# Optimization experiments

Hardware: AMD Instinct MI355X
Metric: run time of the kernel (lower is better)

## Reference

```python
import jax, jax.numpy as jnp
import numpy as np

HID = 1024   # hidden_size
NH = 16      # num_heads
NKV = 4      # num_kv_heads
HD = 64      # head_dim
C = 64       # chunk_size
RATIO = 0.125  # freq_cutoff_ratio
KS = 7       # conv_kernel_size


def setup_inputs() -> dict:
    key = jax.random.key(0)
    ks = jax.random.split(key, 11)
    B, N = 4, 4096
    s = 0.02
    return {
        "hidden_states": jax.random.normal(ks[0], (B, N, HID), jnp.float32),
        "q_w": jax.random.normal(ks[1], (NH * HD, HID), jnp.float32) * s,
        "k_w": jax.random.normal(ks[2], (NKV * HD, HID), jnp.float32) * s,
        "v_w": jax.random.normal(ks[3], (NKV * HD, HID), jnp.float32) * s,
        "o_w": jax.random.normal(ks[4], (HID, NH * HD), jnp.float32) * s,
        "dw_r": jax.random.normal(ks[5], (HID, 1, KS), jnp.float32) * 0.3,
        "pw_r": jax.random.normal(ks[6], (HID, HID), jnp.float32) * s,
        "dw_i": jax.random.normal(ks[7], (HID, 1, KS), jnp.float32) * 0.3,
        "pw_i": jax.random.normal(ks[8], (HID, HID), jnp.float32) * s,
        "gate_w": jax.random.normal(ks[9], (HID, HID), jnp.float32) * s,
        "alpha_raw": jnp.zeros((1,), jnp.float32),
    }


def _block_causal_attention(x, qw, kw, vw, ow, k):
    # x: [B, nc, k, D] real. Flatten chunk freq bins; chunk j attends to chunks 0..j.
    B, nc, _, D = x.shape
    T = nc * k
    xf = x.reshape(B, T, D)
    q = (xf @ qw.T).reshape(B, T, NH, HD).transpose(0, 2, 1, 3)    # [B,H,T,hd]
    kk = (xf @ kw.T).reshape(B, T, NKV, HD).transpose(0, 2, 1, 3)
    v = (xf @ vw.T).reshape(B, T, NKV, HD).transpose(0, 2, 1, 3)
    rep = NH // NKV
    kk = jnp.repeat(kk, rep, axis=1)
    v = jnp.repeat(v, rep, axis=1)
    chunk_ids = jnp.arange(T) // k
    mask = chunk_ids[:, None] >= chunk_ids[None, :]                # [T,T] bool
    scores = jnp.einsum('bhqd,bhkd->bhqk', q, kk) / np.float32(np.sqrt(HD))
    scores = jnp.where(mask[None, None], scores, jnp.finfo(scores.dtype).min)
    p = jax.nn.softmax(scores, axis=-1)
    o = jnp.einsum('bhqk,bhkd->bhqd', p, v)
    o = o.transpose(0, 2, 1, 3).reshape(B, T, NH * HD)
    return (o @ ow.T).reshape(B, nc, k, D)


def _causal_conv(x, dw, pw):
    # x: [B, nc, L, D] real. Depthwise causal conv + GELU + pointwise conv.
    B, nc, L, D = x.shape
    xc = x.reshape(B * nc, L, D).transpose(0, 2, 1)                # [BN, D, L]
    xp = jnp.pad(xc, ((0, 0), (0, 0), (KS - 1, 0)))                # causal left pad
    y = jax.lax.conv_general_dilated(
        xp, dw, window_strides=(1,), padding='VALID',
        dimension_numbers=('NCH', 'OIH', 'NCH'), feature_group_count=D)
    y = jax.nn.gelu(y, approximate=False)
    y = jnp.einsum('ncl,oc->nol', y, pw)                           # 1x1 conv
    return y.transpose(0, 2, 1).reshape(B, nc, L, D)


def _forward(hidden_states, q_w, k_w, v_w, o_w, dw_r, pw_r, dw_i, pw_i, gate_w, alpha_raw):
    B, N, D = hidden_states.shape
    pad_len = (-N) % C
    x = jnp.pad(hidden_states, ((0, 0), (0, pad_len), (0, 0))) if pad_len else hidden_states
    nc = x.shape[1] // C
    chunks = x.reshape(B, nc, C, D)
    Xh = jnp.fft.rfft(chunks.astype(jnp.float32), axis=2)          # [B,nc,M,D] complex
    M = Xh.shape[2]
    k = max(1, int(M * RATIO))
    X_low, X_high = Xh[:, :, :k, :], Xh[:, :, k:, :]
    # low-freq: block-causal attention on real and imag parts separately
    A_r = _block_causal_attention(X_low.real, q_w, k_w, v_w, o_w, k)
    A_i = _block_causal_attention(X_low.imag, q_w, k_w, v_w, o_w, k)
    A_low = jax.lax.complex(A_r, A_i)
    # high-freq: causal conv branch, gated by per-chunk time-domain mean
    H_r = _causal_conv(X_high.real, dw_r, pw_r)
    H_i = _causal_conv(X_high.imag, dw_i, pw_i)
    g = jax.nn.sigmoid(chunks.mean(axis=2) @ gate_w.T)[:, :, None, :]  # [B,nc,1,D]
    A_high = jax.lax.complex(H_r * g, H_i * g) + X_high
    alpha = jax.nn.sigmoid(alpha_raw)                               # [1]
    A_low_fused = alpha * A_low + (1.0 - alpha) * X_low
    Y_hat = jnp.concatenate([A_low_fused, A_high], axis=2)
    Y = jnp.fft.irfft(Y_hat, n=C, axis=2)
    return Y.reshape(B, -1, D)[:, :N, :].astype(hidden_states.dtype)


def reference(hidden_states, q_w, k_w, v_w, o_w, dw_r, pw_r, dw_i, pw_i, gate_w, alpha_raw):
    return _forward(hidden_states, q_w, k_w, v_w, o_w, dw_r, pw_r, dw_i, pw_i, gate_w, alpha_raw)
```

## Files before the change

### kernel.cpp

```cpp
#include <hip/hip_runtime.h>
#include <math.h>


typedef __bf16 bf16_t;
typedef bf16_t bf16x8 __attribute__((ext_vector_type(8)));
typedef float f32x4 __attribute__((ext_vector_type(4)));

#define EP_NONE 0
#define EP_SIGMOID 1
#define EP_FUSELOW 2
#define EP_HIGH 3

__device__ __forceinline__ void gld_lds16(const bf16_t* g, bf16_t* l) {
  __builtin_amdgcn_global_load_lds(
      (const __attribute__((address_space(1))) unsigned int*)g,
      (__attribute__((address_space(3))) unsigned int*)l, 16, 0, 0);
}

__global__ __launch_bounds__(256) void prep_w(
    const float* __restrict__ qw, const float* __restrict__ kw,
    const float* __restrict__ vw, const float* __restrict__ ow,
    const float* __restrict__ gw, const float* __restrict__ pwr,
    const float* __restrict__ pwi, bf16_t* __restrict__ Wqkv,
    bf16_t* __restrict__ owb, bf16_t* __restrict__ gwb,
    bf16_t* __restrict__ pwrb, bf16_t* __restrict__ pwib) {
  int gi = blockIdx.x * 256 + threadIdx.x;
  float4 v;
  bf16_t* o;
  if (gi < 393216) {
    if (gi < 262144) v = ((const float4*)qw)[gi];
    else if (gi < 327680) v = ((const float4*)kw)[gi - 262144];
    else v = ((const float4*)vw)[gi - 327680];
    o = Wqkv + (long)gi * 4;
  } else {
    int j = gi - 393216;
    int sel = j >> 18, off = j & 262143;
    const float* s = sel == 0 ? ow : sel == 1 ? gw : sel == 2 ? pwr : pwi;
    bf16_t* d = sel == 0 ? owb : sel == 1 ? gwb : sel == 2 ? pwrb : pwib;
    v = ((const float4*)s)[off];
    o = d + (long)off * 4;
  }
  o[0] = (bf16_t)v.x; o[1] = (bf16_t)v.y; o[2] = (bf16_t)v.z; o[3] = (bf16_t)v.w;
}

__global__ __launch_bounds__(256) void mk_basis(bf16_t* __restrict__ dhi,
                                                bf16_t* __restrict__ dres,
                                                bf16_t* __restrict__ bhi,
                                                bf16_t* __restrict__ bres,
                                                float* __restrict__ tlow) {
  int idx = blockIdx.x * 256 + threadIdx.x;
  const float TW = 6.283185307179586f / 64.f;
  if (idx < 5120) {
    int r = idx >> 6, k = idx & 63;
    float v = 0.f;
    if (r < 33) {
      v = cosf(TW * (float)((r * k) & 63));
    } else if (r < 66) {
      v = -sinf(TW * (float)(((r - 33) * k) & 63));
    }
    bf16_t h = (bf16_t)v;
    float res = v - (float)h;
    dhi[idx] = h;
    dres[idx] = (bf16_t)res;
  } else if (idx < 9216) {
    int i = idx - 5120;
    int t = i >> 6, k = i & 63;
    float v = 0.f;
    if (k < 28) {
      int ft = ((4 + k) * t) & 63;
      v = 2.f * cosf(TW * (float)ft) * (1.f / 64.f);
    } else if (k == 28) {
      int ft = (32 * t) & 63;
      v = cosf(TW * (float)ft) * (1.f / 64.f);
    } else if (k < 57) {
      int ft = ((k - 25) * t) & 63;
      v = -2.f * sinf(TW * (float)ft) * (1.f / 64.f);
    }
    bf16_t h = (bf16_t)v;
    float res = v - (float)h;
    bhi[i] = h;
    bres[i] = (bf16_t)res;
  } else if (idx < 9728) {
    int i = idx - 9216;
    int t = i >> 3, j = i & 7;
    float v = 0.f;
    if (j == 0) v = 1.f / 64.f;
    else if (j < 7) {
      int f = (j + 1) >> 1;
      int ft = (f * t) & 63;
      float th = TW * (float)ft;
      v = (j & 1) ? 2.f * cosf(th) * (1.f / 64.f)
                  : -2.f * sinf(th) * (1.f / 64.f);
    }
    tlow[i] = v;
  }
}

__global__ __launch_bounds__(128) void dft_mfma(
    const float* __restrict__ X, const bf16_t* __restrict__ dhi,
    const bf16_t* __restrict__ dres, bf16_t* __restrict__ Xh,
    bf16_t* __restrict__ XLr, bf16_t* __restrict__ XLi,
    bf16_t* __restrict__ gmean) {
  const int bc = blockIdx.y;
  const int d0 = blockIdx.x * 128;
  const int tid = threadIdx.x;
  const int lane = tid & 63, wave = tid >> 6;
  const int mr = lane & 15, q = lane >> 4;
  const int wn = wave * 64;

  __shared__ bf16_t Bh[128 * 64];
  __shared__ bf16_t Br[128 * 64];

  {
    const float* xc = X + ((long)bc * 64) * 1024 + d0 + tid;
    float xv[64];
#pragma unroll
    for (int t = 0; t < 64; t++) xv[t] = xc[(long)t * 1024];
    const int sw = tid & 7;
#pragma unroll
    for (int g = 0; g < 8; g++) {
      bf16x8 vh, vr;
#pragma unroll
      for (int i = 0; i < 8; i++) {
        float v = xv[g * 8 + i];
        bf16_t h = (bf16_t)v;
        vh[i] = h;
        vr[i] = (bf16_t)(v - (float)h);
      }
      *(bf16x8*)&Bh[tid * 64 + ((g ^ sw) << 3)] = vh;
      *(bf16x8*)&Br[tid * 64 + ((g ^ sw) << 3)] = vr;
    }
  }
  __syncthreads();

  f32x4 acc[5][4];
#pragma unroll
  for (int i = 0; i < 5; i++)
#pragma unroll
    for (int j = 0; j < 4; j++) acc[i][j] = (f32x4){0.f, 0.f, 0.f, 0.f};

#pragma unroll
  for (int s = 0; s < 2; s++) {
    bf16x8 bh[4], br[4];
#pragma unroll
    for (int ni = 0; ni < 4; ni++) {
      int dcol = wn + ni * 16 + mr;
      int so = (((s * 4 + q) ^ (dcol & 7)) << 3);
      bh[ni] = *(const bf16x8*)&Bh[dcol * 64 + so];
      br[ni] = *(const bf16x8*)&Br[dcol * 64 + so];
    }
#pragma unroll
    for (int mi = 0; mi < 5; mi++) {
      int trow = mi * 16 + mr;
      bf16x8 ah = *(const bf16x8*)&dhi[trow * 64 + (s * 4 + q) * 8];
      bf16x8 ar = *(const bf16x8*)&dres[trow * 64 + (s * 4 + q) * 8];
#pragma unroll
      for (int ni = 0; ni < 4; ni++) {
        acc[mi][ni] = __builtin_amdgcn_mfma_f32_16x16x32_bf16(
            ah, bh[ni], acc[mi][ni], 0, 0, 0);
        acc[mi][ni] = __builtin_amdgcn_mfma_f32_16x16x32_bf16(
            ah, br[ni], acc[mi][ni], 0, 0, 0);
        acc[mi][ni] = __builtin_amdgcn_mfma_f32_16x16x32_bf16(
            ar, bh[ni], acc[mi][ni], 0, 0, 0);
      }
    }
  }

  const int b = bc >> 6, ch = bc & 63;
  bf16_t* xp = Xh + (long)bc * 66 * 1024 + d0;
#pragma unroll
  for (int mi = 0; mi < 5; mi++) {
#pragma unroll
    for (int r = 0; r < 4; r++) {
      int row = mi * 16 + q * 4 + r;
      if (row >= 66) continue;
#pragma unroll
      for (int ni = 0; ni < 4; ni++) {
        int col = wn + ni * 16 + mr;
        float val = acc[mi][ni][r];
        xp[(long)row * 1024 + col] = (bf16_t)val;
        if (row == 0)
          gmean[(long)bc * 1024 + d0 + col] = (bf16_t)(val * (1.f / 64.f));
        if (row < 4)
          XLr[((long)(b * 256 + ch * 4 + row)) * 1024 + d0 + col] = (bf16_t)val;
        if (row >= 33 && row < 37)
          XLi[((long)(b * 256 + ch * 4 + row - 33)) * 1024 + d0 + col] =
              (bf16_t)val;
      }
    }
  }
}

template <int EMODE>
__global__ __launch_bounds__(256, 2) void gemm128(
    const bf16_t* __restrict__ A0, const bf16_t* __restrict__ A1,
    const bf16_t* __restrict__ B0, const bf16_t* __restrict__ B1,
    int N, int ntc, int zc,
    void* __restrict__ C0v, void* __restrict__ C1v,
    const bf16_t* __restrict__ E0, const bf16_t* __restrict__ E1,
    const float* __restrict__ alpha_ptr) {
  constexpr int K = 1024;
  constexpr int NT = 32;
  __shared__ bf16_t lds[4][2][128 * 32];

  const int nwg = gridDim.x;
  const int g = (blockIdx.x & 7) * (nwg >> 3) + (blockIdx.x >> 3);
  const int per_mt = ntc * zc;
  const int mt = g / per_mt, rem = g - mt * per_mt;
  const int nt = rem % ntc, z = rem / ntc;
  const bf16_t* A = z ? A1 : A0;
  const bf16_t* B = z ? B1 : B0;
  void* Cv = z ? C1v : C0v;
  const bf16_t* E = z ? E1 : E0;
  const int m0 = mt * 128, n0 = nt * 128;

  const int tid = threadIdx.x;
  const int lane = tid & 63, wave = tid >> 6;
  const int wm = (wave & 1) * 64, wn = (wave >> 1) * 64;
  const int q = lane >> 4, mr = lane & 15;
  const int srow = tid >> 2, sk8 = (tid & 3) * 8;

  f32x4 acc[4][4];
#pragma unroll
  for (int i = 0; i < 4; i++)
#pragma unroll
    for (int j = 0; j < 4; j++) acc[i][j] = (f32x4){0.f, 0.f, 0.f, 0.f};

  auto stage = [&](int t) {
    const int bi = t & 3;
    const int kb = t * 32;
#pragma unroll
    for (int it = 0; it < 2; it++) {
      gld_lds16(A + (long)(m0 + it * 64 + srow) * K + kb + sk8,
                &lds[bi][0][(it * 256 + wave * 64) * 8]);
      gld_lds16(B + (long)(n0 + it * 64 + srow) * K + kb + sk8,
                &lds[bi][1][(it * 256 + wave * 64) * 8]);
    }
  };

  stage(0);
  stage(1);
  stage(2);

  for (int t = 0; t < NT; t++) {
    if (t < NT - 2)
      asm volatile("s_waitcnt vmcnt(8)" ::: "memory");
    else if (t == NT - 2)
      asm volatile("s_waitcnt vmcnt(4)" ::: "memory");
    else
      asm volatile("s_waitcnt vmcnt(0)" ::: "memory");
    __builtin_amdgcn_sched_barrier(0);
    __builtin_amdgcn_s_barrier();
    if (t + 3 < NT) stage(t + 3);

    const bf16_t* As_ = &lds[t & 3][0][0];
    const bf16_t* Bs_ = &lds[t & 3][1][0];
    bf16x8 bfr[4];
#pragma unroll
    for (int ni = 0; ni < 4; ni++)
      bfr[ni] = *(const bf16x8*)&Bs_[(wn + ni * 16 + mr) * 32 + q * 8];
    __builtin_amdgcn_s_setprio(1);
#pragma unroll
    for (int mi = 0; mi < 4; mi++) {
      bf16x8 af = *(const bf16x8*)&As_[(wm + mi * 16 + mr) * 32 + q * 8];
#pragma unroll
      for (int ni = 0; ni < 4; ni++)
        acc[mi][ni] = __builtin_amdgcn_mfma_f32_16x16x32_bf16(
            af, bfr[ni], acc[mi][ni], 0, 0, 0);
    }
    __builtin_amdgcn_s_setprio(0);
  }

  float alpha = 0.f;
  if constexpr (EMODE == EP_FUSELOW) alpha = 1.f / (1.f + __expf(-alpha_ptr[0]));
#pragma unroll
  for (int mi = 0; mi < 4; mi++) {
#pragma unroll
    for (int ni = 0; ni < 4; ni++) {
      int col = n0 + wn + ni * 16 + mr;
      int rbase = m0 + wm + mi * 16 + q * 4;
#pragma unroll
      for (int r = 0; r < 4; r++) {
        int row = rbase + r;
        float val = acc[mi][ni][r];
        if constexpr (EMODE == EP_NONE) {
          ((bf16_t*)Cv)[(long)row * N + col] = (bf16_t)val;
        } else if constexpr (EMODE == EP_SIGMOID) {
          ((float*)Cv)[(long)row * N + col] = 1.f / (1.f + __expf(-val));
        } else {
          float xl = (float)E[(long)row * 1024 + col];
          ((float*)Cv)[(long)row * 1024 + col] = alpha * val + (1.f - alpha) * xl;
        }
      }
    }
  }
}

__global__ __launch_bounds__(512, 2) void gemm256_high(
    const bf16_t* __restrict__ A0, const bf16_t* __restrict__ A1,
    const bf16_t* __restrict__ B0, const bf16_t* __restrict__ B1,
    bf16_t* __restrict__ XhMut, const float* __restrict__ gate) {
  constexpr int K = 1024;
  constexpr int NT = K / 32;
  __shared__ bf16_t lds[4][2][256 * 32];

  const int id = blockIdx.x;
  const int kk = (id & 7) * 29 + (id >> 3);
  const int mt = kk >> 3, rem = kk & 7;
  const int nt = rem & 3, z = rem >> 2;
  const bf16_t* A = z ? A1 : A0;
  const bf16_t* B = z ? B1 : B0;
  const int imoff = z ? 33 * 1024 : 0;
  const int m0 = mt * 256, n0 = nt * 256;

  const int tid = threadIdx.x;
  const int lane = tid & 63, wave = tid >> 6;
  const int wm = (wave & 1) * 128, wn = (wave >> 1) * 64;
  const int q = lane >> 4, mr = lane & 15;
  const int srow = tid >> 2;
  const int gk8 = (((tid & 3) ^ ((((tid >> 2) & 3) + ((tid >> 4) & 3)) & 3)) << 3);

  f32x4 acc[8][4];
#pragma unroll
  for (int i = 0; i < 8; i++)
#pragma unroll
    for (int j = 0; j < 4; j++) acc[i][j] = (f32x4){0.f, 0.f, 0.f, 0.f};

  auto stage = [&](int t) {
    const int bi = t & 3;
    const int kb = t * 32;
#pragma unroll
    for (int rd = 0; rd < 2; rd++) {
      gld_lds16(A + (long)(m0 + rd * 128 + srow) * K + kb + gk8,
                &lds[bi][0][(rd * 512 + wave * 64) * 8]);
      gld_lds16(B + (long)(n0 + rd * 128 + srow) * K + kb + gk8,
                &lds[bi][1][(rd * 512 + wave * 64) * 8]);
    }
  };

  stage(0);
  stage(1);
  stage(2);

  const int asl = (q ^ (((mr & 3) + ((mr >> 2) & 3)) & 3)) * 8;

  for (int t = 0; t < NT; t++) {
    if (t < NT - 2)
      asm volatile("s_waitcnt vmcnt(8)" ::: "memory");
    else if (t == NT - 2)
      asm volatile("s_waitcnt vmcnt(4)" ::: "memory");
    else
      asm volatile("s_waitcnt vmcnt(0)" ::: "memory");
    __builtin_amdgcn_sched_barrier(0);
    __builtin_amdgcn_s_barrier();
    if (t + 3 < NT) stage(t + 3);

    const bf16_t* As_ = &lds[t & 3][0][0];
    const bf16_t* Bs_ = &lds[t & 3][1][0];
    bf16x8 bfr[4];
#pragma unroll
    for (int ni = 0; ni < 4; ni++)
      bfr[ni] = *(const bf16x8*)&Bs_[(wn + ni * 16 + mr) * 32 + asl];
    __builtin_amdgcn_s_setprio(1);
#pragma unroll
    for (int mi = 0; mi < 8; mi++) {
      bf16x8 af = *(const bf16x8*)&As_[(wm + mi * 16 + mr) * 32 + asl];
#pragma unroll
      for (int ni = 0; ni < 4; ni++)
        acc[mi][ni] = __builtin_amdgcn_mfma_f32_16x16x32_bf16(
            af, bfr[ni], acc[mi][ni], 0, 0, 0);
    }
    __builtin_amdgcn_s_setprio(0);
  }

#pragma unroll
  for (int mi = 0; mi < 8; mi++) {
#pragma unroll
    for (int r = 0; r < 4; r++) {
      int row = m0 + wm + mi * 16 + q * 4 + r;
      int bc = row / 29, l = row - bc * 29;
      long xbase = ((long)bc * 66 + 4 + l) * 1024 + imoff;
      const float* gp = gate + (long)bc * 1024;
#pragma unroll
      for (int ni = 0; ni < 4; ni++) {
        int col = n0 + wn + ni * 16 + mr;
        long x = xbase + col;
        XhMut[x] = (bf16_t)fmaf(acc[mi][ni][r], gp[col], (float)XhMut[x]);
      }
    }
  }
}

__global__ __launch_bounds__(256) void attn_mfma(const bf16_t* __restrict__ QKVr,
                                                 const bf16_t* __restrict__ QKVi,
                                                 bf16_t* __restrict__ Or_,
                                                 bf16_t* __restrict__ Oi_) {
  const int h = blockIdx.x;
  const int b = blockIdx.y >> 2, qt = blockIdx.y & 3;
  const bf16_t* QKV = blockIdx.z ? QKVi : QKVr;
  bf16_t* O = blockIdx.z ? Oi_ : Or_;
  const int kvh = h >> 2;
  const int tid = threadIdx.x;
  const int lane = tid & 63, wave = tid >> 6;
  const int mr = lane & 15, q4 = lane >> 4;

  __shared__ bf16_t Ks[64 * 72];
  __shared__ bf16_t Vt[64 * 72];
  __shared__ bf16_t Ps[4][16 * 72];

  bf16x8 af[2];
  {
    const bf16_t* qp =
        QKV + (long)(b * 256 + qt * 64 + wave * 16 + mr) * 1536 + h * 64;
    af[0] = *(const bf16x8*)(qp + q4 * 8);
    af[1] = *(const bf16x8*)(qp + 32 + q4 * 8);
  }
  f32x4 Oacc[4];
#pragma unroll
  for (int ni = 0; ni < 4; ni++) Oacc[ni] = (f32x4){0.f, 0.f, 0.f, 0.f};
  float mrow[4], lrow[4];
#pragma unroll
  for (int r = 0; r < 4; r++) { mrow[r] = -1e30f; lrow[r] = 0.f; }

  for (int kt = 0; kt <= qt; kt++) {
#pragma unroll
    for (int it = 0; it < 2; it++) {
      int idx = tid + it * 256;
      int key = idx >> 3, dg = idx & 7;
      const bf16_t* kp = QKV + (long)(b * 256 + kt * 64 + key) * 1536 + 1024 +
                         kvh * 64 + dg * 8;
      *(bf16x8*)&Ks[key * 72 + dg * 8] = *(const bf16x8*)kp;
      bf16x8 vv = *(const bf16x8*)(kp + 256);
#pragma unroll
      for (int j = 0; j < 8; j++) Vt[(dg * 8 + j) * 72 + key] = vv[j];
    }
    __syncthreads();

    f32x4 S[4];
#pragma unroll
    for (int ni = 0; ni < 4; ni++) {
      S[ni] = (f32x4){0.f, 0.f, 0.f, 0.f};
#pragma unroll
      for (int s = 0; s < 2; s++) {
        bf16x8 kb = *(const bf16x8*)&Ks[(ni * 16 + mr) * 72 + s * 32 + q4 * 8];
        S[ni] = __builtin_amdgcn_mfma_f32_16x16x32_bf16(af[s], kb, S[ni], 0, 0, 0);
      }
    }
#pragma unroll
    for (int ni = 0; ni < 4; ni++) {
#pragma unroll
      for (int r = 0; r < 4; r++) {
        float v = S[ni][r] * 0.125f;
        if (kt == qt) {
          int qrow = wave * 16 + q4 * 4 + r;
          int kcol = ni * 16 + mr;
          if ((qrow >> 2) < (kcol >> 2)) v = -1e30f;
        }
        S[ni][r] = v;
      }
    }
#pragma unroll
    for (int r = 0; r < 4; r++) {
      float mx = fmaxf(fmaxf(S[0][r], S[1][r]), fmaxf(S[2][r], S[3][r]));
#pragma unroll
      for (int off = 1; off < 16; off <<= 1) mx = fmaxf(mx, __shfl_xor(mx, off));
      float mn = fmaxf(mrow[r], mx);
      float sc = __expf(mrow[r] - mn);
      mrow[r] = mn;
      float rs = 0.f;
#pragma unroll
      for (int ni = 0; ni < 4; ni++) {
        float p = __expf(S[ni][r] - mn);
        rs += p;
        Ps[wave][(q4 * 4 + r) * 72 + ni * 16 + mr] = (bf16_t)p;
      }
#pragma unroll
      for (int off = 1; off < 16; off <<= 1) rs += __shfl_xor(rs, off);
      lrow[r] = lrow[r] * sc + rs;
#pragma unroll
      for (int ni = 0; ni < 4; ni++) Oacc[ni][r] *= sc;
    }
    bf16x8 pa[2];
    pa[0] = *(const bf16x8*)&Ps[wave][mr * 72 + q4 * 8];
    pa[1] = *(const bf16x8*)&Ps[wave][mr * 72 + 32 + q4 * 8];
#pragma unroll
    for (int ni = 0; ni < 4; ni++) {
#pragma unroll
      for (int s = 0; s < 2; s++) {
        bf16x8 vb = *(const bf16x8*)&Vt[(ni * 16 + mr) * 72 + s * 32 + q4 * 8];
        Oacc[ni] = __builtin_amdgcn_mfma_f32_16x16x32_bf16(pa[s], vb, Oacc[ni], 0, 0, 0);
      }
    }
    __syncthreads();
  }

#pragma unroll
  for (int r = 0; r < 4; r++) {
    float inv = 1.f / lrow[r];
    long row = b * 256 + qt * 64 + wave * 16 + q4 * 4 + r;
#pragma unroll
    for (int ni = 0; ni < 4; ni++)
      O[row * 1024 + h * 64 + ni * 16 + mr] = (bf16_t)(Oacc[ni][r] * inv);
  }
}

__global__ __launch_bounds__(256) void dwconv_kernel(const bf16_t* __restrict__ Xh,
                                                     const float* __restrict__ dwr,
                                                     const float* __restrict__ dwi,
                                                     bf16_t* __restrict__ Gr,
                                                     bf16_t* __restrict__ Gi) {
  const int d = blockIdx.x * 256 + threadIdx.x;
  const int bc = blockIdx.y;
  const float* dw = blockIdx.z ? dwi : dwr;
  bf16_t* G = blockIdx.z ? Gi : Gr;
  const int imoff = blockIdx.z ? 33 * 1024 : 0;
  float w[7];
#pragma unroll
  for (int j = 0; j < 7; j++) w[j] = dw[d * 7 + j];
  float x[29];
#pragma unroll
  for (int l = 0; l < 29; l++)
    x[l] = (float)Xh[((long)bc * 66 + 4 + l) * 1024 + imoff + d];
#pragma unroll
  for (int l = 0; l < 29; l++) {
    float y = 0.f;
#pragma unroll
    for (int j = 0; j < 7; j++) {
      int src = l - 6 + j;
      if (src >= 0) y = fmaf(w[j], x[src], y);
    }
    float ge = 0.5f * y * (1.f + erff(y * 0.7071067811865475f));
    G[((long)bc * 29 + l) * 1024 + d] = (bf16_t)ge;
  }
}

__global__ __launch_bounds__(128) void irfft_mfma(
    const bf16_t* __restrict__ Xh, const float* __restrict__ Afr,
    const float* __restrict__ Afi, const bf16_t* __restrict__ bhi,
    const bf16_t* __restrict__ bres, const float* __restrict__ tlow,
    float* __restrict__ out) {
  const int bc = blockIdx.y;
  const int d0 = blockIdx.x * 128;
  const int tid = threadIdx.x;
  const int lane = tid & 63, wave = tid >> 6;
  const int mr = lane & 15, q = lane >> 4;
  const int wn = wave * 64;

  __shared__ bf16_t Bs[128 * 64];
  __shared__ float Tl[64 * 8];

  ((float4*)Tl)[tid] = ((const float4*)tlow)[tid];

  {
    const bf16_t* xc = Xh + (long)bc * 66 * 1024 + d0 + tid;
    bf16_t xv[57];
#pragma unroll
    for (int j = 0; j < 57; j++) {
      int row = (j < 29) ? (4 + j) : (8 + j);
      xv[j] = xc[(long)row * 1024];
    }
    const int sw = tid & 7;
#pragma unroll
    for (int g = 0; g < 8; g++) {
      bf16x8 v;
#pragma unroll
      for (int i = 0; i < 8; i++) {
        int j = g * 8 + i;
        v[i] = (j < 57) ? xv[j] : (bf16_t)0.f;
      }
      *(bf16x8*)&Bs[tid * 64 + ((g ^ sw) << 3)] = v;
    }
  }
  __syncthreads();

  f32x4 acc[4][4];
#pragma unroll
  for (int i = 0; i < 4; i++)
#pragma unroll
    for (int j = 0; j < 4; j++) acc[i][j] = (f32x4){0.f, 0.f, 0.f, 0.f};

#pragma unroll
  for (int s = 0; s < 2; s++) {
    bf16x8 bfv[4];
#pragma unroll
    for (int ni = 0; ni < 4; ni++) {
      int dcol = wn + ni * 16 + mr;
      bfv[ni] = *(const bf16x8*)&Bs[dcol * 64 + (((s * 4 + q) ^ (dcol & 7)) << 3)];
    }
#pragma unroll
    for (int mi = 0; mi < 4; mi++) {
      int trow = mi * 16 + mr;
      bf16x8 ah = *(const bf16x8*)&bhi[trow * 64 + (s * 4 + q) * 8];
      bf16x8 ar = *(const bf16x8*)&bres[trow * 64 + (s * 4 + q) * 8];
#pragma unroll
      for (int ni = 0; ni < 4; ni++) {
        acc[mi][ni] = __builtin_amdgcn_mfma_f32_16x16x32_bf16(
            ah, bfv[ni], acc[mi][ni], 0, 0, 0);
        acc[mi][ni] = __builtin_amdgcn_mfma_f32_16x16x32_bf16(
            ar, bfv[ni], acc[mi][ni], 0, 0, 0);
      }
    }
  }

  const int arow = (bc >> 6) * 256 + (bc & 63) * 4;
  float R[4][7];
#pragma unroll
  for (int ni = 0; ni < 4; ni++) {
    long ab = (long)arow * 1024 + d0 + wn + ni * 16 + mr;
    R[ni][0] = Afr[ab];
    R[ni][1] = Afr[ab + 1024];
    R[ni][2] = Afi[ab + 1024];
    R[ni][3] = Afr[ab + 2048];
    R[ni][4] = Afi[ab + 2048];
    R[ni][5] = Afr[ab + 3072];
    R[ni][6] = Afi[ab + 3072];
  }
  const long obase = ((long)bc * 64) * 1024 + d0;
#pragma unroll
  for (int mi = 0; mi < 4; mi++) {
#pragma unroll
    for (int r = 0; r < 4; r++) {
      int t = mi * 16 + q * 4 + r;
      const float* tl = &Tl[t * 8];
#pragma unroll
      for (int ni = 0; ni < 4; ni++) {
        float low = tl[0] * R[ni][0];
        low = fmaf(tl[1], R[ni][1], low);
        low = fmaf(tl[2], R[ni][2], low);
        low = fmaf(tl[3], R[ni][3], low);
        low = fmaf(tl[4], R[ni][4], low);
        low = fmaf(tl[5], R[ni][5], low);
        low = fmaf(tl[6], R[ni][6], low);
        out[obase + (long)t * 1024 + wn + ni * 16 + mr] = acc[mi][ni][r] + low;
      }
    }
  }
}

extern "C" void kernel_launch(void* const* d_in, const int* in_sizes, int n_in,
                              void* d_out, int out_size, void* d_ws, size_t ws_size,
                              hipStream_t stream) {
  const float* hidden = (const float*)d_in[0];
  const float* q_w = (const float*)d_in[1];
  const float* k_w = (const float*)d_in[2];
  const float* v_w = (const float*)d_in[3];
  const float* o_w = (const float*)d_in[4];
  const float* dw_r = (const float*)d_in[5];
  const float* pw_r = (const float*)d_in[6];
  const float* dw_i = (const float*)d_in[7];
  const float* pw_i = (const float*)d_in[8];
  const float* gate_w = (const float*)d_in[9];
  const float* alpha_raw = (const float*)d_in[10];
  float* out = (float*)d_out;

  float* ws = (float*)d_ws;
  float* Afr = ws;
  float* Afi = Afr + 1048576;
  float* gg = Afi + 1048576;
  bf16_t* bws = (bf16_t*)(gg + 262144);
  bf16_t* Xh = bws;
  bf16_t* Wqkv_b = Xh + 17301504;
  bf16_t* ow_b = Wqkv_b + 1572864;
  bf16_t* gw_b = ow_b + 1048576;
  bf16_t* pwr_b = gw_b + 1048576;
  bf16_t* pwi_b = pwr_b + 1048576;
  bf16_t* XLr = pwi_b + 1048576;
  bf16_t* XLi = XLr + 1048576;
  bf16_t* gmean = XLi + 1048576;
  bf16_t* QKVbr = gmean + 262144;
  bf16_t* QKVbi = QKVbr + 1572864;
  bf16_t* Obr = QKVbi + 1572864;
  bf16_t* Obi = Obr + 1048576;
  bf16_t* Gr = Obi + 1048576;
  bf16_t* Gi = Gr + 7602176;
  bf16_t* bhi = Gi + 7602176;
  bf16_t* bres = bhi + 4096;
  bf16_t* dbhi = bres + 4096;
  bf16_t* dbres = dbhi + 5120;
  float* tlowp = (float*)(dbres + 5120);

  mk_basis<<<38, 256, 0, stream>>>(dbhi, dbres, bhi, bres, tlowp);
  dft_mfma<<<dim3(8, 256), 128, 0, stream>>>(hidden, dbhi, dbres, Xh, XLr,
                                             XLi, gmean);
  prep_w<<<5632, 256, 0, stream>>>(q_w, k_w, v_w, o_w, gate_w, pw_r, pw_i,
                                   Wqkv_b, ow_b, gw_b, pwr_b, pwi_b);
  gemm128<EP_NONE><<<192, 256, 0, stream>>>(
      XLr, XLi, Wqkv_b, Wqkv_b, 1536, 12, 2, QKVbr, QKVbi, nullptr, nullptr,
      nullptr);
  gemm128<EP_SIGMOID><<<16, 256, 0, stream>>>(
      gmean, gmean, gw_b, gw_b, 1024, 8, 1, gg, gg, nullptr, nullptr,
      nullptr);
  attn_mfma<<<dim3(16, 16, 2), 256, 0, stream>>>(QKVbr, QKVbi, Obr, Obi);
  gemm128<EP_FUSELOW><<<128, 256, 0, stream>>>(
      Obr, Obi, ow_b, ow_b, 1024, 8, 2, Afr, Afi, XLr, XLi, alpha_raw);
  dwconv_kernel<<<dim3(4, 256, 2), 256, 0, stream>>>(Xh, dw_r, dw_i, Gr, Gi);
  gemm256_high<<<dim3(232), 512, 0, stream>>>(Gr, Gi, pwr_b, pwi_b, Xh, gg);
  irfft_mfma<<<dim3(8, 256), 128, 0, stream>>>(Xh, Afr, Afi, bhi, bres,
                                               tlowp, out);
}
```

Measured before the change: 330.5 us.

## Restructure high-freq GEMM into BK=64 double-buffered ping-pong with split staging

Rewrites the gemm256_high main loop to use 64-wide K tiles with two LDS buffers instead of four 32-wide buffers. Each iteration is split into four MFMA phases separated by barriers, and the next tile's global-to-LDS loads are interleaved in halves between phases. It also switches to an XOR-8 swizzle for the wider rows. The goal is fewer loop iterations and better overlap of loads with MFMA. The cost is more barriers per iteration and a shallower prefetch depth.

```diff
diff --git a/kernel.cpp b/kernel.cpp
--- a/kernel.cpp
+++ b/kernel.cpp
@@ -301,15 +301,15 @@
     const bf16_t* __restrict__ B0, const bf16_t* __restrict__ B1,
     bf16_t* __restrict__ XhMut, const float* __restrict__ gate) {
   constexpr int K = 1024;
-  constexpr int NT = K / 32;
-  __shared__ bf16_t lds[4][2][256 * 32];
+  constexpr int NT = 16;
+  __shared__ bf16_t lds[2][2][256 * 64];
 
   const int id = blockIdx.x;
   const int kk = (id & 7) * 29 + (id >> 3);
   const int mt = kk >> 3, rem = kk & 7;
   const int nt = rem & 3, z = rem >> 2;
-  const bf16_t* A = z ? A1 : A0;
-  const bf16_t* B = z ? B1 : B0;
+  const bf16_t* A = (z ? A1 : A0) + (long)(mt * 256) * K;
+  const bf16_t* B = (z ? B1 : B0) + (long)(nt * 256) * K;
   const int imoff = z ? 33 * 1024 : 0;
   const int m0 = mt * 256, n0 = nt * 256;
 
@@ -317,8 +317,9 @@
   const int lane = tid & 63, wave = tid >> 6;
   const int wm = (wave & 1) * 128, wn = (wave >> 1) * 64;
   const int q = lane >> 4, mr = lane & 15;
-  const int srow = tid >> 2;
-  const int gk8 = (((tid & 3) ^ ((((tid >> 2) & 3) + ((tid >> 4) & 3)) & 3)) << 3);
+  const int sw = mr & 7;
+  const int sl0 = ((q ^ sw) << 3);
+  const int sl1 = (((4 + q) ^ sw) << 3);
 
   f32x4 acc[8][4];
 #pragma unroll
@@ -326,51 +327,102 @@
 #pragma unroll
     for (int j = 0; j < 4; j++) acc[i][j] = (f32x4){0.f, 0.f, 0.f, 0.f};
 
-  auto stage = [&](int t) {
-    const int bi = t & 3;
-    const int kb = t * 32;
+  auto stage_half = [&](int t, int mat, int h) {
+    const bf16_t* src = mat ? B : A;
+    bf16_t* dst = &lds[t & 1][mat][0];
+    const int kb = t * 64;
 #pragma unroll
     for (int rd = 0; rd < 2; rd++) {
-      gld_lds16(A + (long)(m0 + rd * 128 + srow) * K + kb + gk8,
-                &lds[bi][0][(rd * 512 + wave * 64) * 8]);
-      gld_lds16(B + (long)(n0 + rd * 128 + srow) * K + kb + gk8,
-                &lds[bi][1][(rd * 512 + wave * 64) * 8]);
+      const int c = rd * 512 + tid;
+      const int row = h * 128 + (c >> 3);
+      const int gs = (c & 7) ^ (row & 7);
+      gld_lds16(src + (long)row * K + kb + gs * 8,
+                dst + (h * 1024 + rd * 512 + wave * 64) * 8);
     }
   };
 
-  stage(0);
-  stage(1);
-  stage(2);
-
-  const int asl = (q ^ (((mr & 3) + ((mr >> 2) & 3)) & 3)) * 8;
+  stage_half(0, 0, 0); stage_half(0, 0, 1);
+  stage_half(0, 1, 0); stage_half(0, 1, 1);
+  asm volatile("s_waitcnt vmcnt(0)" ::: "memory");
+  __builtin_amdgcn_sched_barrier(0);
+  __builtin_amdgcn_s_barrier();
 
   for (int t = 0; t < NT; t++) {
-    if (t < NT - 2)
-      asm volatile("s_waitcnt vmcnt(8)" ::: "memory");
-    else if (t == NT - 2)
-      asm volatile("s_waitcnt vmcnt(4)" ::: "memory");
-    else
-      asm volatile("s_waitcnt vmcnt(0)" ::: "memory");
+    const bf16_t* As_ = &lds[t & 1][0][0];
+    const bf16_t* Bs_ = &lds[t & 1][1][0];
+    const bool st = (t + 1 < NT);
+    bf16x8 afr[4], bfr[4];
+
+#pragma unroll
+    for (int i = 0; i < 4; i++) {
+      afr[i] = *(const bf16x8*)&As_[(wm + i * 16 + mr) * 64 + sl0];
+      bfr[i] = *(const bf16x8*)&Bs_[(wn + i * 16 + mr) * 64 + sl0];
+    }
+    if (st) { stage_half(t + 1, 0, 0); stage_half(t + 1, 1, 0); }
+    __builtin_amdgcn_s_barrier();
+    asm volatile("s_waitcnt lgkmcnt(0)" ::: "memory");
     __builtin_amdgcn_sched_barrier(0);
-    __builtin_amdgcn_s_barrier();
-    if (t + 3 < NT) stage(t + 3);
-
-    const bf16_t* As_ = &lds[t & 3][0][0];
-    const bf16_t* Bs_ = &lds[t & 3][1][0];
-    bf16x8 bfr[4];
-#pragma unroll
-    for (int ni = 0; ni < 4; ni++)
-      bfr[ni] = *(const bf16x8*)&Bs_[(wn + ni * 16 + mr) * 32 + asl];
     __builtin_amdgcn_s_setprio(1);
 #pragma unroll
-    for (int mi = 0; mi < 8; mi++) {
-      bf16x8 af = *(const bf16x8*)&As_[(wm + mi * 16 + mr) * 32 + asl];
-#pragma unroll
-      for (int ni = 0; ni < 4; ni++)
-        acc[mi][ni] = __builtin_amdgcn_mfma_f32_16x16x32_bf16(
-            af, bfr[ni], acc[mi][ni], 0, 0, 0);
-    }
+    for (int i = 0; i < 4; i++)
+#pragma unroll
+      for (int n2 = 0; n2 < 4; n2++)
+        acc[i][n2] = __builtin_amdgcn_mfma_f32_16x16x32_bf16(
+            afr[i], bfr[n2], acc[i][n2], 0, 0, 0);
     __builtin_amdgcn_s_setprio(0);
+    __builtin_amdgcn_s_barrier();
+
+#pragma unroll
+    for (int i = 0; i < 4; i++)
+      afr[i] = *(const bf16x8*)&As_[(wm + (4 + i) * 16 + mr) * 64 + sl0];
+    if (st) { stage_half(t + 1, 0, 1); stage_half(t + 1, 1, 1); }
+    __builtin_amdgcn_s_barrier();
+    asm volatile("s_waitcnt lgkmcnt(0)" ::: "memory");
+    __builtin_amdgcn_sched_barrier(0);
+    __builtin_amdgcn_s_setprio(1);
+#pragma unroll
+    for (int i = 0; i < 4; i++)
+#pragma unroll
+      for (int n2 = 0; n2 < 4; n2++)
+        acc[4 + i][n2] = __builtin_amdgcn_mfma_f32_16x16x32_bf16(
+            afr[i], bfr[n2], acc[4 + i][n2], 0, 0, 0);
+    __builtin_amdgcn_s_setprio(0);
+    __builtin_amdgcn_s_barrier();
+
+#pragma unroll
+    for (int i = 0; i < 4; i++) {
+      afr[i] = *(const bf16x8*)&As_[(wm + i * 16 + mr) * 64 + sl1];
+      bfr[i] = *(const bf16x8*)&Bs_[(wn + i * 16 + mr) * 64 + sl1];
+    }
+    __builtin_amdgcn_s_barrier();
+    asm volatile("s_waitcnt lgkmcnt(0)" ::: "memory");
+    __builtin_amdgcn_sched_barrier(0);
+    __builtin_amdgcn_s_setprio(1);
+#pragma unroll
+    for (int i = 0; i < 4; i++)
+#pragma unroll
+      for (int n2 = 0; n2 < 4; n2++)
+        acc[i][n2] = __builtin_amdgcn_mfma_f32_16x16x32_bf16(
+            afr[i], bfr[n2], acc[i][n2], 0, 0, 0);
+    __builtin_amdgcn_s_setprio(0);
+    __builtin_amdgcn_s_barrier();
+
+#pragma unroll
+    for (int i = 0; i < 4; i++)
+      afr[i] = *(const bf16x8*)&As_[(wm + (4 + i) * 16 + mr) * 64 + sl1];
+    __builtin_amdgcn_s_barrier();
+    asm volatile("s_waitcnt lgkmcnt(0)" ::: "memory");
+    __builtin_amdgcn_sched_barrier(0);
+    __builtin_amdgcn_s_setprio(1);
+#pragma unroll
+    for (int i = 0; i < 4; i++)
+#pragma unroll
+      for (int n2 = 0; n2 < 4; n2++)
+        acc[4 + i][n2] = __builtin_amdgcn_mfma_f32_16x16x32_bf16(
+            afr[i], bfr[n2], acc[4 + i][n2], 0, 0, 0);
+    __builtin_amdgcn_s_setprio(0);
+    if (st) asm volatile("s_waitcnt vmcnt(0)" ::: "memory");
+    __builtin_amdgcn_s_barrier();
   }
 
 #pragma unroll
```

Result: faster. 316.6 us (-4.2%).
